# Kernel optimization log

Hardware: AMD Instinct MI355X
Metric: run time of the kernel (lower is better)

Reference implementation:

```python
import jax, jax.numpy as jnp
from jax import lax
import numpy as np

V, E, H, L, C = 50257, 128, 128, 2, 32
B, T = 64, 2048


def setup_inputs() -> dict:
    key = jax.random.key(0)
    ks = jax.random.split(key, 12)
    s_e = 1.0 / np.sqrt(H)  # torch GRU init scale
    inp = {
        'x': jax.random.randint(ks[0], (B, T), 0, V),
        'emb': jax.random.normal(ks[1], (V, E), jnp.float32),
        'w_ih0': jax.random.uniform(ks[2], (3 * H, E), jnp.float32, -s_e, s_e),
        'w_hh0': jax.random.uniform(ks[3], (3 * H, H), jnp.float32, -s_e, s_e),
        'b_ih0': jax.random.uniform(ks[4], (3 * H,), jnp.float32, -s_e, s_e),
        'b_hh0': jax.random.uniform(ks[5], (3 * H,), jnp.float32, -s_e, s_e),
        'w_ih1': jax.random.uniform(ks[6], (3 * H, H), jnp.float32, -s_e, s_e),
        'w_hh1': jax.random.uniform(ks[7], (3 * H, H), jnp.float32, -s_e, s_e),
        'b_ih1': jax.random.uniform(ks[8], (3 * H,), jnp.float32, -s_e, s_e),
        'b_hh1': jax.random.uniform(ks[9], (3 * H,), jnp.float32, -s_e, s_e),
        'fc_w': jax.random.uniform(ks[10], (C, H), jnp.float32, -s_e, s_e),
        'fc_b': jax.random.uniform(ks[11], (C,), jnp.float32, -s_e, s_e),
    }
    return inp


def _gru_layer(x_tbe, w_ih, w_hh, b_ih, b_hh):
    # x_tbe: [T, B, Din]; torch GRU gate order: r, z, n
    gi = jnp.einsum('tbd,gd->tbg', x_tbe, w_ih) + b_ih  # [T, B, 3H] precomputed input gates
    h0 = jnp.zeros((x_tbe.shape[1], w_hh.shape[0] // 3), x_tbe.dtype)

    def step(h, gi_t):
        gh = h @ w_hh.T + b_hh
        ir, iz, inn = jnp.split(gi_t, 3, axis=-1)
        hr, hz, hn = jnp.split(gh, 3, axis=-1)
        r = jax.nn.sigmoid(ir + hr)
        z = jax.nn.sigmoid(iz + hz)
        n = jnp.tanh(inn + r * hn)
        h_new = (1.0 - z) * n + z * h
        return h_new, h_new

    _, ys = lax.scan(step, h0, gi)
    return ys  # [T, B, H]


def reference(x, emb, w_ih0, w_hh0, b_ih0, b_hh0, w_ih1, w_hh1, b_ih1, b_hh1, fc_w, fc_b):
    e = emb[x]                      # [B, T, E] embedding lookup
    h = jnp.swapaxes(e, 0, 1)       # [T, B, E] (time-major for scan)
    h = _gru_layer(h, w_ih0, w_hh0, b_ih0, b_hh0)
    h = _gru_layer(h, w_ih1, w_hh1, b_ih1, b_hh1)
    y = jnp.swapaxes(h, 0, 1)       # [B, T, H]
    out = jax.nn.relu(y @ fc_w.T + fc_b)  # [B, T, C]
    return out.reshape(-1, out.shape[-1])  # [B*T, C]
```

## Files before the change

kernel.cpp:

```cpp
#include <hip/hip_runtime.h>
#include <math.h>

#define B_ 64
#define T_ 2048
#define E_ 128
#define H_ 128
#define G3_ 384
#define C_ 32
#define M_ (T_ * B_)
#define CH_ 16
#define NCH_ (T_ / CH_)

typedef _Float16 f16x2 __attribute__((ext_vector_type(2)));

__device__ __forceinline__ f16x2 as_h2(unsigned int u) {
    union { unsigned int u; f16x2 h; } c; c.u = u; return c.h;
}

#if __has_builtin(__builtin_amdgcn_fdot2)
__device__ __forceinline__ float fdot2_acc(f16x2 a, f16x2 b, float c) {
    return __builtin_amdgcn_fdot2(a, b, c, false);
}
#else
__device__ __forceinline__ float fdot2_acc(f16x2 a, f16x2 b, float c) {
    return fmaf((float)a.y, (float)b.y, fmaf((float)a.x, (float)b.x, c));
}
#endif

__device__ __forceinline__ void wait_ge(int* f, int need) {
    while (__hip_atomic_load(f, __ATOMIC_ACQUIRE, __HIP_MEMORY_SCOPE_AGENT) < need)
        __builtin_amdgcn_s_sleep(8);
}

template <bool GATHER>
__global__ __launch_bounds__(384, 1) void gates_gemm(
    const float* __restrict__ src,
    const int*   __restrict__ xidx,
    const float* __restrict__ w,
    const float* __restrict__ bias,
    float* __restrict__ gi)
{
    const int r = threadIdx.x;
    f16x2 wr[64];
    {
        const float2* w2 = (const float2*)(w + (long)r * 128);
#pragma unroll
        for (int i = 0; i < 64; i++) {
            float2 v = w2[i];
            wr[i] = (f16x2){(_Float16)v.x, (_Float16)v.y};
        }
    }
    const float br = bias[r];

    __shared__ __align__(16) f16x2 rows[8][64];

    for (int grp = blockIdx.x; grp < M_ / 8; grp += gridDim.x) {
        const int m0 = grp * 8;
        __syncthreads();
        for (int j = r; j < 512; j += 384) {
            const int s = j >> 6;
            const int p = j & 63;
            const int mm = m0 + s;
            long row;
            if (GATHER) {
                const int t = mm >> 6;
                const int bb = mm & 63;
                row = (long)xidx[bb * T_ + t];
            } else {
                row = mm;
            }
            float2 v = ((const float2*)(src + row * 128))[p];
            rows[s][p] = (f16x2){(_Float16)v.x, (_Float16)v.y};
        }
        __syncthreads();
        for (int s = 0; s < 8; s++) {
            const uint4* h16 = (const uint4*)rows[s];
            float a0 = br, a1 = 0.f, a2 = 0.f, a3 = 0.f;
#pragma unroll
            for (int i = 0; i < 16; i++) {
                uint4 u = h16[i];
                a0 = fdot2_acc(wr[4*i+0], as_h2(u.x), a0);
                a1 = fdot2_acc(wr[4*i+1], as_h2(u.y), a1);
                a2 = fdot2_acc(wr[4*i+2], as_h2(u.z), a2);
                a3 = fdot2_acc(wr[4*i+3], as_h2(u.w), a3);
            }
            gi[(long)(m0 + s) * G3_ + r] = (a0 + a1) + (a2 + a3);
        }
    }
}

#define DOT96(HSRC, S0, S1, S2)                                                \
  {                                                                            \
    float a00 = 0.f, a01 = 0.f, a10 = 0.f, a11 = 0.f, a20 = 0.f, a21 = 0.f;    \
    _Pragma("unroll")                                                          \
    for (int i = 0; i < 8; i++) {                                              \
      uint4 u = (HSRC)[i];                                                     \
      f16x2 ux = as_h2(u.x), uy = as_h2(u.y), uz = as_h2(u.z), uw = as_h2(u.w);\
      a00 = fdot2_acc(wr[0][4*i+0], ux, a00);                                  \
      a10 = fdot2_acc(wr[1][4*i+0], ux, a10);                                  \
      a20 = fdot2_acc(wr[2][4*i+0], ux, a20);                                  \
      a01 = fdot2_acc(wr[0][4*i+1], uy, a01);                                  \
      a11 = fdot2_acc(wr[1][4*i+1], uy, a11);                                  \
      a21 = fdot2_acc(wr[2][4*i+1], uy, a21);                                  \
      a00 = fdot2_acc(wr[0][4*i+2], uz, a00);                                  \
      a10 = fdot2_acc(wr[1][4*i+2], uz, a10);                                  \
      a20 = fdot2_acc(wr[2][4*i+2], uz, a20);                                  \
      a01 = fdot2_acc(wr[0][4*i+3], uw, a01);                                  \
      a11 = fdot2_acc(wr[1][4*i+3], uw, a11);                                  \
      a21 = fdot2_acc(wr[2][4*i+3], uw, a21);                                  \
    }                                                                          \
    S0 = a00 + a01; S1 = a10 + a11; S2 = a20 + a21;                            \
  }

#define GSTEPX(CUR, NXT, IR, IZ, INN, TT, TP)                                  \
  {                                                                            \
    const uint4* hsrc = (const uint4*)((const char*)hb[CUR] + kh * 128);       \
    float s0, s1, s2;                                                          \
    DOT96(hsrc, s0, s1, s2);                                                   \
    const float hr = s0 + __shfl_xor(s0, 1) + bg0;                             \
    const float hz = s1 + __shfl_xor(s1, 1) + bg1;                             \
    const float hn = s2 + __shfl_xor(s2, 1) + bg2;                             \
    const float rr = 1.f / (1.f + __expf(-((IR) + hr)));                       \
    const float zz = 1.f / (1.f + __expf(-((IZ) + hz)));                       \
    const float na = (INN) + rr * hn;                                          \
    const float nn = 1.f - 2.f / (__expf(2.f * na) + 1.f);                     \
    h_own = (1.f - zz) * nn + zz * h_own;                                      \
    if (kh == 0) hb[NXT][g] = (_Float16)h_own;                                 \
    else         y_g[(size_t)(TT) * (B_ * H_)] = h_own;                        \
    {                                                                          \
      const int tp = ((TP) < T_) ? (TP) : (TT);                                \
      const float* gp = gi_g + (size_t)tp * (B_ * G3_);                        \
      IR = gp[0]; IZ = gp[128]; INN = gp[256];                                 \
    }                                                                          \
    asm volatile("s_waitcnt lgkmcnt(0)" ::: "memory");                         \
    __builtin_amdgcn_s_barrier();                                              \
    __builtin_amdgcn_sched_barrier(0);                                         \
  }

__global__ __launch_bounds__(256, 1) void gru_pipe(
    float* __restrict__ gi,
    const float* __restrict__ w_hh0,
    const float* __restrict__ b_hh0,
    const float* __restrict__ w_ih1,
    const float* __restrict__ b_ih1,
    const float* __restrict__ w_hh1,
    const float* __restrict__ b_hh1,
    float* __restrict__ ybuf,
    int* __restrict__ flags)
{
    const int tid = threadIdx.x;
    const int w   = tid >> 6;
    const int l   = tid & 63;
    const int g   = w * 32 + (l >> 1);
    const int kh  = l & 1;
    const int role = blockIdx.x >> 6;
    const int b    = blockIdx.x & 63;
    int* p0 = flags + b;
    int* p1 = flags + 64 + b;

    __shared__ __align__(16) _Float16 hb[2][128];
    __shared__ __align__(16) f16x2 yrow[16][64];

    if (role == 1) {
        f16x2 wr[3][32];
#pragma unroll
        for (int G = 0; G < 3; G++) {
            const float2* w2 = (const float2*)(w_ih1 + (size_t)(g + 128 * G) * 128 + kh * 64);
#pragma unroll
            for (int i = 0; i < 32; i++) {
                float2 v = w2[i];
                wr[G][i] = (f16x2){(_Float16)v.x, (_Float16)v.y};
            }
        }
        const float c0 = b_ih1[g], c1 = b_ih1[g + 128], c2 = b_ih1[g + 256];

        for (int c = 0; c < NCH_; c++) {
            if (tid == 0) wait_ge(p0, (c + 1) * CH_);
            __syncthreads();
            for (int j = tid; j < 16 * 64; j += 256) {
                const int s = j >> 6, p = j & 63;
                const float2 v = ((const float2*)(ybuf +
                    ((size_t)(c * CH_ + s) * B_ + b) * H_))[p];
                yrow[s][p] = (f16x2){(_Float16)v.x, (_Float16)v.y};
            }
            __syncthreads();
            for (int s = 0; s < 16; s++) {
                const uint4* hsrc = (const uint4*)yrow[s] + kh * 8;
                float s0, s1, s2;
                DOT96(hsrc, s0, s1, s2);
                const float r0v = s0 + __shfl_xor(s0, 1);
                const float r1v = s1 + __shfl_xor(s1, 1);
                const float r2v = s2 + __shfl_xor(s2, 1);
                if (kh == 0) {
                    float* go = gi + ((size_t)(c * CH_ + s) * B_ + b) * G3_ + g;
                    go[0]   = r0v + c0;
                    go[128] = r1v + c1;
                    go[256] = r2v + c2;
                }
            }
            asm volatile("s_waitcnt vmcnt(0)" ::: "memory");
            __syncthreads();
            if (tid == 0)
                __hip_atomic_store(p1, c + 1, __ATOMIC_RELEASE, __HIP_MEMORY_SCOPE_AGENT);
        }
        return;
    }

    const float* wsrc = (role == 2) ? w_hh1 : w_hh0;
    const float* bsrc = (role == 2) ? b_hh1 : b_hh0;

    f16x2 wr[3][32];
#pragma unroll
    for (int G = 0; G < 3; G++) {
        const float2* w2 = (const float2*)(wsrc + (size_t)(g + 128 * G) * 128 + kh * 64);
#pragma unroll
        for (int i = 0; i < 32; i++) {
            float2 v = w2[i];
            wr[G][i] = (f16x2){(_Float16)v.x, (_Float16)v.y};
        }
    }
    const float bg0 = bsrc[g];
    const float bg1 = bsrc[g + 128];
    const float bg2 = bsrc[g + 256];

    if (tid < 128) hb[0][tid] = (_Float16)0.f;
    float h_own = 0.f;

    const float* gi_g = gi + (size_t)b * G3_ + g;
    float* y_g = ybuf + (size_t)b * H_ + g;

    if (role == 2) {
        if (tid == 0) wait_ge(p1, 2);
        __syncthreads();
    }

    float irA = gi_g[0], izA = gi_g[128], innA = gi_g[256];
    const float* pp1 = gi_g + (size_t)(B_ * G3_);
    float irB = pp1[0], izB = pp1[128], innB = pp1[256];

    __syncthreads();

    for (int c = 0; c < NCH_; c++) {
        if (role == 2) {
            const int need = (c + 2 < NCH_) ? (c + 2) : NCH_;
            if (tid == 0) wait_ge(p1, need);
            __syncthreads();
        }
        const int t0 = c * CH_;
        for (int i = 0; i < CH_ / 2; i++) {
            const int t = t0 + 2 * i;
            GSTEPX(0, 1, irA, izA, innA, t,     t + 2)
            GSTEPX(1, 0, irB, izB, innB, t + 1, t + 3)
        }
        if (role == 0) {
            asm volatile("s_waitcnt vmcnt(0)" ::: "memory");
            __syncthreads();
            if (tid == 0)
                __hip_atomic_store(p0, (c + 1) * CH_, __ATOMIC_RELEASE, __HIP_MEMORY_SCOPE_AGENT);
        }
    }
}

__global__ __launch_bounds__(256, 2) void fc_relu(
    const float* __restrict__ y,
    const float* __restrict__ fc_w,
    const float* __restrict__ fc_b,
    float* __restrict__ out)
{
    const int tid = threadIdx.x;
    const int c = tid & 31;
    const int slot = tid >> 5;

    float4 wr[32];
    const float4* w4 = (const float4*)(fc_w + c * 128);
#pragma unroll
    for (int i = 0; i < 32; i++) wr[i] = w4[i];
    const float bc = fc_b[c];

    __shared__ __align__(16) float rows[8][128];

    for (int grp = blockIdx.x; grp < M_ / 8; grp += gridDim.x) {
        const int m0 = grp * 8;
        __syncthreads();
        for (int i = tid; i < 8 * 128; i += 256) {
            rows[i >> 7][i & 127] = y[(long)m0 * 128 + i];
        }
        __syncthreads();
        const float4* h4 = (const float4*)rows[slot];
        float a0 = bc, a1 = 0.f, a2 = 0.f, a3 = 0.f;
#pragma unroll
        for (int i = 0; i < 32; i += 4) {
            float4 h0 = h4[i], h1 = h4[i + 1], h2 = h4[i + 2], h3 = h4[i + 3];
            a0 = fmaf(wr[i].w, h0.w, fmaf(wr[i].z, h0.z, fmaf(wr[i].y, h0.y, fmaf(wr[i].x, h0.x, a0))));
            a1 = fmaf(wr[i+1].w, h1.w, fmaf(wr[i+1].z, h1.z, fmaf(wr[i+1].y, h1.y, fmaf(wr[i+1].x, h1.x, a1))));
            a2 = fmaf(wr[i+2].w, h2.w, fmaf(wr[i+2].z, h2.z, fmaf(wr[i+2].y, h2.y, fmaf(wr[i+2].x, h2.x, a2))));
            a3 = fmaf(wr[i+3].w, h3.w, fmaf(wr[i+3].z, h3.z, fmaf(wr[i+3].y, h3.y, fmaf(wr[i+3].x, h3.x, a3))));
        }
        float acc = (a0 + a1) + (a2 + a3);
        acc = fmaxf(acc, 0.f);
        const int m = m0 + slot;
        const int t = m >> 6;
        const int b = m & 63;
        out[((long)b * T_ + t) * C_ + c] = acc;
    }
}

extern "C" void kernel_launch(void* const* d_in, const int* in_sizes, int n_in,
                              void* d_out, int out_size, void* d_ws, size_t ws_size,
                              hipStream_t stream) {
    const int*   x     = (const int*)d_in[0];
    const float* emb   = (const float*)d_in[1];
    const float* w_ih0 = (const float*)d_in[2];
    const float* w_hh0 = (const float*)d_in[3];
    const float* b_ih0 = (const float*)d_in[4];
    const float* b_hh0 = (const float*)d_in[5];
    const float* w_ih1 = (const float*)d_in[6];
    const float* w_hh1 = (const float*)d_in[7];
    const float* b_ih1 = (const float*)d_in[8];
    const float* b_hh1 = (const float*)d_in[9];
    const float* fc_w  = (const float*)d_in[10];
    const float* fc_b  = (const float*)d_in[11];
    float* out = (float*)d_out;

    float* gi   = (float*)d_ws;
    float* ybuf = (float*)((char*)d_ws + (size_t)M_ * G3_ * sizeof(float));

    hipMemsetAsync(d_out, 0, 128 * sizeof(int), stream);

    gates_gemm<true><<<512, 384, 0, stream>>>(emb, x, w_ih0, b_ih0, gi);
    gru_pipe<<<192, 256, 0, stream>>>(gi, w_hh0, b_hh0, w_ih1, b_ih1, w_hh1, b_hh1,
                                      ybuf, (int*)d_out);
    fc_relu<<<512, 256, 0, stream>>>(ybuf, fc_w, fc_b, out);
}
```

Before: 1.704 ms.

## Fuse layer-0 input-gate GEMM into the pipelined GRU kernel as a producer role

Removes the separate gates_gemm launch and adds a fourth role to gru_pipe: producer blocks that gather embedding rows and compute layer-0 input gates chunk by chunk, signalling a new flag that the layer-0 recurrence blocks wait on. This overlaps the embedding gather and input projection with the recurrence instead of running them serially beforehand. The cost is 256 co-resident blocks instead of 192, extra flag spin-waits on layer 0, and reliance on every block being resident at once to avoid deadlock.

```diff
diff --git a/kernel.cpp b/kernel.cpp
--- a/kernel.cpp
+++ b/kernel.cpp
@@ -30,63 +30,6 @@
 __device__ __forceinline__ void wait_ge(int* f, int need) {
     while (__hip_atomic_load(f, __ATOMIC_ACQUIRE, __HIP_MEMORY_SCOPE_AGENT) < need)
         __builtin_amdgcn_s_sleep(8);
-}
-
-template <bool GATHER>
-__global__ __launch_bounds__(384, 1) void gates_gemm(
-    const float* __restrict__ src,
-    const int*   __restrict__ xidx,
-    const float* __restrict__ w,
-    const float* __restrict__ bias,
-    float* __restrict__ gi)
-{
-    const int r = threadIdx.x;
-    f16x2 wr[64];
-    {
-        const float2* w2 = (const float2*)(w + (long)r * 128);
-#pragma unroll
-        for (int i = 0; i < 64; i++) {
-            float2 v = w2[i];
-            wr[i] = (f16x2){(_Float16)v.x, (_Float16)v.y};
-        }
-    }
-    const float br = bias[r];
-
-    __shared__ __align__(16) f16x2 rows[8][64];
-
-    for (int grp = blockIdx.x; grp < M_ / 8; grp += gridDim.x) {
-        const int m0 = grp * 8;
-        __syncthreads();
-        for (int j = r; j < 512; j += 384) {
-            const int s = j >> 6;
-            const int p = j & 63;
-            const int mm = m0 + s;
-            long row;
-            if (GATHER) {
-                const int t = mm >> 6;
-                const int bb = mm & 63;
-                row = (long)xidx[bb * T_ + t];
-            } else {
-                row = mm;
-            }
-            float2 v = ((const float2*)(src + row * 128))[p];
-            rows[s][p] = (f16x2){(_Float16)v.x, (_Float16)v.y};
-        }
-        __syncthreads();
-        for (int s = 0; s < 8; s++) {
-            const uint4* h16 = (const uint4*)rows[s];
-            float a0 = br, a1 = 0.f, a2 = 0.f, a3 = 0.f;
-#pragma unroll
-            for (int i = 0; i < 16; i++) {
-                uint4 u = h16[i];
-                a0 = fdot2_acc(wr[4*i+0], as_h2(u.x), a0);
-                a1 = fdot2_acc(wr[4*i+1], as_h2(u.y), a1);
-                a2 = fdot2_acc(wr[4*i+2], as_h2(u.z), a2);
-                a3 = fdot2_acc(wr[4*i+3], as_h2(u.w), a3);
-            }
-            gi[(long)(m0 + s) * G3_ + r] = (a0 + a1) + (a2 + a3);
-        }
-    }
 }
 
 #define DOT96(HSRC, S0, S1, S2)                                                \
@@ -138,6 +81,10 @@
   }
 
 __global__ __launch_bounds__(256, 1) void gru_pipe(
+    const float* __restrict__ emb,
+    const int*   __restrict__ xidx,
+    const float* __restrict__ w_ih0,
+    const float* __restrict__ b_ih0,
     float* __restrict__ gi,
     const float* __restrict__ w_hh0,
     const float* __restrict__ b_hh0,
@@ -155,37 +102,48 @@
     const int kh  = l & 1;
     const int role = blockIdx.x >> 6;
     const int b    = blockIdx.x & 63;
-    int* p0 = flags + b;
-    int* p1 = flags + 64 + b;
+    int* q0 = flags + b;
+    int* p0 = flags + 64 + b;
+    int* p1 = flags + 128 + b;
 
     __shared__ __align__(16) _Float16 hb[2][128];
-    __shared__ __align__(16) f16x2 yrow[16][64];
-
-    if (role == 1) {
+    __shared__ __align__(16) f16x2 srow[16][64];
+
+    if (role == 0 || role == 2) {
+        const float* wsrc = (role == 0) ? w_ih0 : w_ih1;
+        const float* bsrc = (role == 0) ? b_ih0 : b_ih1;
         f16x2 wr[3][32];
 #pragma unroll
         for (int G = 0; G < 3; G++) {
-            const float2* w2 = (const float2*)(w_ih1 + (size_t)(g + 128 * G) * 128 + kh * 64);
+            const float2* w2 = (const float2*)(wsrc + (size_t)(g + 128 * G) * 128 + kh * 64);
 #pragma unroll
             for (int i = 0; i < 32; i++) {
                 float2 v = w2[i];
                 wr[G][i] = (f16x2){(_Float16)v.x, (_Float16)v.y};
             }
         }
-        const float c0 = b_ih1[g], c1 = b_ih1[g + 128], c2 = b_ih1[g + 256];
+        const float c0 = bsrc[g], c1 = bsrc[g + 128], c2 = bsrc[g + 256];
 
         for (int c = 0; c < NCH_; c++) {
-            if (tid == 0) wait_ge(p0, (c + 1) * CH_);
+            if (role == 2) {
+                if (tid == 0) wait_ge(p0, (c + 1) * CH_);
+            }
             __syncthreads();
             for (int j = tid; j < 16 * 64; j += 256) {
                 const int s = j >> 6, p = j & 63;
-                const float2 v = ((const float2*)(ybuf +
-                    ((size_t)(c * CH_ + s) * B_ + b) * H_))[p];
-                yrow[s][p] = (f16x2){(_Float16)v.x, (_Float16)v.y};
+                const float* src;
+                if (role == 0) {
+                    const long row = (long)xidx[b * T_ + c * CH_ + s];
+                    src = emb + row * 128;
+                } else {
+                    src = ybuf + ((size_t)(c * CH_ + s) * B_ + b) * H_;
+                }
+                const float2 v = ((const float2*)src)[p];
+                srow[s][p] = (f16x2){(_Float16)v.x, (_Float16)v.y};
             }
             __syncthreads();
             for (int s = 0; s < 16; s++) {
-                const uint4* hsrc = (const uint4*)yrow[s] + kh * 8;
+                const uint4* hsrc = (const uint4*)srow[s] + kh * 8;
                 float s0, s1, s2;
                 DOT96(hsrc, s0, s1, s2);
                 const float r0v = s0 + __shfl_xor(s0, 1);
@@ -200,14 +158,17 @@
             }
             asm volatile("s_waitcnt vmcnt(0)" ::: "memory");
             __syncthreads();
-            if (tid == 0)
-                __hip_atomic_store(p1, c + 1, __ATOMIC_RELEASE, __HIP_MEMORY_SCOPE_AGENT);
+            if (tid == 0) {
+                int* rel = (role == 0) ? q0 : p1;
+                __hip_atomic_store(rel, c + 1, __ATOMIC_RELEASE, __HIP_MEMORY_SCOPE_AGENT);
+            }
         }
         return;
     }
 
-    const float* wsrc = (role == 2) ? w_hh1 : w_hh0;
-    const float* bsrc = (role == 2) ? b_hh1 : b_hh0;
+    const float* wsrc = (role == 3) ? w_hh1 : w_hh0;
+    const float* bsrc = (role == 3) ? b_hh1 : b_hh0;
+    int* wf = (role == 3) ? p1 : q0;
 
     f16x2 wr[3][32];
 #pragma unroll
@@ -229,10 +190,8 @@
     const float* gi_g = gi + (size_t)b * G3_ + g;
     float* y_g = ybuf + (size_t)b * H_ + g;
 
-    if (role == 2) {
-        if (tid == 0) wait_ge(p1, 2);
-        __syncthreads();
-    }
+    if (tid == 0) wait_ge(wf, 2);
+    __syncthreads();
 
     float irA = gi_g[0], izA = gi_g[128], innA = gi_g[256];
     const float* pp1 = gi_g + (size_t)(B_ * G3_);
@@ -241,18 +200,16 @@
     __syncthreads();
 
     for (int c = 0; c < NCH_; c++) {
-        if (role == 2) {
-            const int need = (c + 2 < NCH_) ? (c + 2) : NCH_;
-            if (tid == 0) wait_ge(p1, need);
-            __syncthreads();
-        }
+        const int need = (c + 2 < NCH_) ? (c + 2) : NCH_;
+        if (tid == 0) wait_ge(wf, need);
+        __syncthreads();
         const int t0 = c * CH_;
         for (int i = 0; i < CH_ / 2; i++) {
             const int t = t0 + 2 * i;
             GSTEPX(0, 1, irA, izA, innA, t,     t + 2)
             GSTEPX(1, 0, irB, izB, innB, t + 1, t + 3)
         }
-        if (role == 0) {
+        if (role == 1) {
             asm volatile("s_waitcnt vmcnt(0)" ::: "memory");
             __syncthreads();
             if (tid == 0)
@@ -325,10 +282,10 @@
     float* gi   = (float*)d_ws;
     float* ybuf = (float*)((char*)d_ws + (size_t)M_ * G3_ * sizeof(float));
 
-    hipMemsetAsync(d_out, 0, 128 * sizeof(int), stream);
-
-    gates_gemm<true><<<512, 384, 0, stream>>>(emb, x, w_ih0, b_ih0, gi);
-    gru_pipe<<<192, 256, 0, stream>>>(gi, w_hh0, b_hh0, w_ih1, b_ih1, w_hh1, b_hh1,
+    hipMemsetAsync(d_out, 0, 192 * sizeof(int), stream);
+
+    gru_pipe<<<256, 256, 0, stream>>>(emb, x, w_ih0, b_ih0, gi,
+                                      w_hh0, b_hh0, w_ih1, b_ih1, w_hh1, b_hh1,
                                       ybuf, (int*)d_out);
     fc_relu<<<512, 256, 0, stream>>>(ybuf, fc_w, fc_b, out);
 }
```

Measured after the change: 1.727 ms. About the same (+1.4%).

## Compute layer-0 input gates with MFMA 16x16x32 f16 instead of fdot2

Applied to the files above, without the earlier changes.

Replaces the fdot2-based gather+GEMM for layer-0 input gates with an MFMA kernel. Each block handles one third of the 384 gate outputs for a stripe of 16-row groups, keeps weight fragments in registers, and reads gathered embedding rows from an XOR-swizzled LDS tile. The goal is to cut ALU time in the input projection by using matrix cores, at the cost of more blocks and a different output-write pattern. The recurrent GRU pipeline probably dominates total time, so the end-to-end effect may be limited.

```diff
diff --git a/kernel.cpp b/kernel.cpp
--- a/kernel.cpp
+++ b/kernel.cpp
@@ -12,6 +12,8 @@
 #define NCH_ (T_ / CH_)
 
 typedef _Float16 f16x2 __attribute__((ext_vector_type(2)));
+typedef _Float16 f16x8 __attribute__((ext_vector_type(8)));
+typedef float f32x4 __attribute__((ext_vector_type(4)));
 
 __device__ __forceinline__ f16x2 as_h2(unsigned int u) {
     union { unsigned int u; f16x2 h; } c; c.u = u; return c.h;
@@ -32,60 +34,71 @@
         __builtin_amdgcn_s_sleep(8);
 }
 
-template <bool GATHER>
-__global__ __launch_bounds__(384, 1) void gates_gemm(
-    const float* __restrict__ src,
+__global__ __launch_bounds__(256, 1) void gates_mfma(
+    const float* __restrict__ emb,
     const int*   __restrict__ xidx,
     const float* __restrict__ w,
     const float* __restrict__ bias,
     float* __restrict__ gi)
 {
-    const int r = threadIdx.x;
-    f16x2 wr[64];
-    {
-        const float2* w2 = (const float2*)(w + (long)r * 128);
-#pragma unroll
-        for (int i = 0; i < 64; i++) {
-            float2 v = w2[i];
-            wr[i] = (f16x2){(_Float16)v.x, (_Float16)v.y};
-        }
-    }
-    const float br = bias[r];
-
-    __shared__ __align__(16) f16x2 rows[8][64];
-
-    for (int grp = blockIdx.x; grp < M_ / 8; grp += gridDim.x) {
-        const int m0 = grp * 8;
-        __syncthreads();
-        for (int j = r; j < 512; j += 384) {
+    const int tid = threadIdx.x;
+    const int q   = tid >> 6;
+    const int l   = tid & 63;
+    const int rl  = l & 15;
+    const int kg  = l >> 4;
+    const int ob  = blockIdx.x % 3;
+    const int stripe = blockIdx.x / 3;
+    const int obase  = ob * 128 + q * 32;
+
+    f16x8 aF[2][4];
+#pragma unroll
+    for (int p = 0; p < 2; p++) {
+        const float* wrow = w + (size_t)(obase + p * 16 + rl) * 128 + kg * 8;
+#pragma unroll
+        for (int ks = 0; ks < 4; ks++) {
+            const f32x4 lo = *(const f32x4*)(wrow + ks * 32);
+            const f32x4 hi = *(const f32x4*)(wrow + ks * 32 + 4);
+            aF[p][ks] = (f16x8){(_Float16)lo[0], (_Float16)lo[1], (_Float16)lo[2], (_Float16)lo[3],
+                                (_Float16)hi[0], (_Float16)hi[1], (_Float16)hi[2], (_Float16)hi[3]};
+        }
+    }
+    f32x4 bv[2];
+#pragma unroll
+    for (int p = 0; p < 2; p++)
+#pragma unroll
+        for (int r = 0; r < 4; r++)
+            bv[p][r] = bias[obase + p * 16 + 4 * kg + r];
+
+    __shared__ __align__(16) char rows[4096];
+
+    for (int g = stripe; g < M_ / 16; g += 512) {
+        const int m0 = g * 16;
+        __syncthreads();
+#pragma unroll
+        for (int k = 0; k < 4; k++) {
+            const int j = tid + 256 * k;
             const int s = j >> 6;
-            const int p = j & 63;
+            const int p2 = j & 63;
             const int mm = m0 + s;
-            long row;
-            if (GATHER) {
-                const int t = mm >> 6;
-                const int bb = mm & 63;
-                row = (long)xidx[bb * T_ + t];
-            } else {
-                row = mm;
-            }
-            float2 v = ((const float2*)(src + row * 128))[p];
-            rows[s][p] = (f16x2){(_Float16)v.x, (_Float16)v.y};
-        }
-        __syncthreads();
-        for (int s = 0; s < 8; s++) {
-            const uint4* h16 = (const uint4*)rows[s];
-            float a0 = br, a1 = 0.f, a2 = 0.f, a3 = 0.f;
-#pragma unroll
-            for (int i = 0; i < 16; i++) {
-                uint4 u = h16[i];
-                a0 = fdot2_acc(wr[4*i+0], as_h2(u.x), a0);
-                a1 = fdot2_acc(wr[4*i+1], as_h2(u.y), a1);
-                a2 = fdot2_acc(wr[4*i+2], as_h2(u.z), a2);
-                a3 = fdot2_acc(wr[4*i+3], as_h2(u.w), a3);
-            }
-            gi[(long)(m0 + s) * G3_ + r] = (a0 + a1) + (a2 + a3);
-        }
+            const int t = mm >> 6;
+            const int bb = mm & 63;
+            const long row = (long)xidx[bb * T_ + t];
+            const float2 v = ((const float2*)(emb + row * 128))[p2];
+            const int byte = (s * 256 + p2 * 4) ^ ((s & 7) << 4);
+            *(f16x2*)(rows + byte) = (f16x2){(_Float16)v.x, (_Float16)v.y};
+        }
+        __syncthreads();
+        f32x4 acc0 = bv[0], acc1 = bv[1];
+#pragma unroll
+        for (int ks = 0; ks < 4; ks++) {
+            const int byte = (rl * 256 + ks * 64 + kg * 16) ^ ((rl & 7) << 4);
+            const f16x8 bf = *(const f16x8*)(rows + byte);
+            acc0 = __builtin_amdgcn_mfma_f32_16x16x32_f16(aF[0][ks], bf, acc0, 0, 0, 0);
+            acc1 = __builtin_amdgcn_mfma_f32_16x16x32_f16(aF[1][ks], bf, acc1, 0, 0, 0);
+        }
+        float* go = gi + (size_t)(m0 + rl) * G3_ + obase + 4 * kg;
+        *(f32x4*)(go)      = acc0;
+        *(f32x4*)(go + 16) = acc1;
     }
 }
 
@@ -327,7 +340,7 @@
 
     hipMemsetAsync(d_out, 0, 128 * sizeof(int), stream);
 
-    gates_gemm<true><<<512, 384, 0, stream>>>(emb, x, w_ih0, b_ih0, gi);
+    gates_mfma<<<1536, 256, 0, stream>>>(emb, x, w_ih0, b_ih0, gi);
     gru_pipe<<<192, 256, 0, stream>>>(gi, w_hh0, b_hh0, w_ih1, b_ih1, w_hh1, b_hh1,
                                       ybuf, (int*)d_out);
     fc_relu<<<512, 256, 0, stream>>>(ybuf, fc_w, fc_b, out);
```

Result: faster. 1.524 ms (-10.6%).
